# Optimization experiments

Hardware: AMD Instinct MI355X
Metric: run time of the kernel (lower is better)

The kernel has to match this reference:

```python
import jax, jax.numpy as jnp
import numpy as np

EPS = 1e-8  # matches torch.nn.functional.cosine_similarity default eps


def setup_inputs() -> dict:
    key = jax.random.key(0)
    k1, k2 = jax.random.split(key)
    B, C, L, D = 65536, 64, 64, 128
    x = jax.random.normal(k1, (B, D), dtype=jnp.float32)
    category_embeddings = jax.random.normal(k2, (C, L, D), dtype=jnp.float32)
    leaf_usage_counts = jnp.zeros((C, L), dtype=jnp.float32)
    return {
        "x": x,
        "category_embeddings": category_embeddings,
        "leaf_usage_counts": leaf_usage_counts,
    }


def reference(x, category_embeddings, leaf_usage_counts):
    # Cosine similarity: [B, C, L] without materializing the broadcast [B,C,L,D].
    x_norm = jnp.maximum(jnp.linalg.norm(x, axis=-1, keepdims=True), EPS)        # [B, 1]
    e_norm = jnp.maximum(jnp.linalg.norm(category_embeddings, axis=-1), EPS)     # [C, L]
    dots = jnp.einsum('bd,cld->bcl', x, category_embeddings)                     # [B, C, L]
    cosine_sim = dots / (x_norm[:, :, None] * e_norm[None, :, :])                # [B, C, L]

    # Training-path usage-count update (done under no_grad in torch):
    # per-category bincount of argmax leaf, scatter-added into the buffer.
    max_indices = jnp.argmax(cosine_sim, axis=2)                                 # [B, C] int
    C, L = leaf_usage_counts.shape
    cat_ids = jnp.broadcast_to(jnp.arange(C)[None, :], max_indices.shape)        # [B, C]
    leaf_counts = jnp.zeros((C, L), jnp.float32).at[cat_ids, max_indices].add(1.0)
    new_leaf_usage_counts = leaf_usage_counts + leaf_counts                      # [C, L]

    cosine_sim_max = jnp.max(cosine_sim, axis=2)                                 # [B, C]
    return cosine_sim_max, new_leaf_usage_counts
```

## Files before the change

### kernel.cpp

```cpp
#include <hip/hip_runtime.h>
#include <stdint.h>
#include <stddef.h>

#define D      128
#define NCATS  64
#define NLEAF  64
#define NC_BLK 4
#define BM     512
#define BIAS   32.0f

typedef _Float16 half8_t  __attribute__((ext_vector_type(8)));
typedef _Float16 half4h_t __attribute__((ext_vector_type(4)));
typedef float    float4_t __attribute__((ext_vector_type(4)));

__device__ __forceinline__ void async_ld16(const void* g, void* l) {
  __builtin_amdgcn_global_load_lds((const __attribute__((address_space(1))) uint32_t*)g,
                                   (__attribute__((address_space(3))) uint32_t*)l,
                                   16, 0, 0);
}

__global__ __launch_bounds__(256) void prep_e_kernel(const float* __restrict__ e,
                                                     char* __restrict__ e16,
                                                     const float* __restrict__ cin,
                                                     float* __restrict__ counts_out) {
  const int t  = threadIdx.x;
  const int rl = t >> 4;
  const int cc = t & 15;
  const int row = blockIdx.x * 16 + rl;
  const float* src = e + (size_t)row * D + cc * 8;
  float4_t v0 = *(const float4_t*)src;
  float4_t v1 = *(const float4_t*)(src + 4);
  float ss = v0.x*v0.x + v0.y*v0.y + v0.z*v0.z + v0.w*v0.w +
             v1.x*v1.x + v1.y*v1.y + v1.z*v1.z + v1.w*v1.w;
  ss += __shfl_xor(ss, 1);
  ss += __shfl_xor(ss, 2);
  ss += __shfl_xor(ss, 4);
  ss += __shfl_xor(ss, 8);
  const float inv = 1.0f / fmaxf(sqrtf(ss), 1e-8f);
  half8_t h;
  h[0] = (_Float16)(v0.x * inv); h[1] = (_Float16)(v0.y * inv);
  h[2] = (_Float16)(v0.z * inv); h[3] = (_Float16)(v0.w * inv);
  h[4] = (_Float16)(v1.x * inv); h[5] = (_Float16)(v1.y * inv);
  h[6] = (_Float16)(v1.z * inv); h[7] = (_Float16)(v1.w * inv);
  const int dc = cc ^ (rl & 7);
  *(half8_t*)(e16 + (size_t)row * 256 + dc * 16) = h;
  if (blockIdx.x < (NCATS * NLEAF) / 256)
    counts_out[blockIdx.x * 256 + t] = cin[blockIdx.x * 256 + t];
}

__global__ __launch_bounds__(512, 3) void main_kernel(const float* __restrict__ x,
                                                      const char* __restrict__ e16,
                                                      float* __restrict__ cos_out,
                                                      float* __restrict__ counts_out) {
  __shared__ __align__(16) char ebuf[NC_BLK][16384];
  __shared__ unsigned hist[NC_BLK * NLEAF];
  __shared__ __align__(16) _Float16 stage[BM * NC_BLK];

  const int tid  = threadIdx.x;
  const int w    = tid >> 6;
  const int lane = tid & 63;
  const int q    = lane >> 4;
  const int wl   = lane & 15;

  const int xcd    = blockIdx.x & 7;
  const int rb     = xcd * 16 + ((blockIdx.x >> 3) & 15);
  const int c_base = (blockIdx.x >> 7) * NC_BLK;
  const int b_base = rb * BM;

  {
    const char* g = e16 + (size_t)(c_base + (w >> 1)) * 16384 + (w & 1) * 8192 + lane * 16;
    char* l = &ebuf[w >> 1][(w & 1) * 8192 + lane * 16];
#pragma unroll
    for (int j = 0; j < 8; ++j) async_ld16(g + j * 1024, l + j * 1024);
  }

  for (int i = tid; i < NC_BLK * NLEAF; i += 512) hist[i] = 0;

  half8_t bfrag[4][4];
  float inv_x[4];
#pragma unroll
  for (int nt = 0; nt < 4; ++nt) {
    const int row = b_base + w * 64 + nt * 16 + wl;
    const float* xr = x + (size_t)row * D;
    float ss = 0.f;
#pragma unroll
    for (int s = 0; s < 4; ++s) {
      const float* p = xr + s * 32 + q * 8;
      float4_t v0 = *(const float4_t*)p;
      float4_t v1 = *(const float4_t*)(p + 4);
      half8_t h;
      h[0] = (_Float16)v0.x; h[1] = (_Float16)v0.y;
      h[2] = (_Float16)v0.z; h[3] = (_Float16)v0.w;
      h[4] = (_Float16)v1.x; h[5] = (_Float16)v1.y;
      h[6] = (_Float16)v1.z; h[7] = (_Float16)v1.w;
      bfrag[nt][s] = h;
      ss += v0.x*v0.x + v0.y*v0.y + v0.z*v0.z + v0.w*v0.w +
            v1.x*v1.x + v1.y*v1.y + v1.z*v1.z + v1.w*v1.w;
    }
    ss += __shfl_xor(ss, 16);
    ss += __shfl_xor(ss, 32);
    inv_x[nt] = 1.0f / fmaxf(sqrtf(ss), 1e-8f);
  }

  int rowbase[4], xoff[4];
#pragma unroll
  for (int rt = 0; rt < 4; ++rt) rowbase[rt] = (rt * 16 + wl) * 256;
#pragma unroll
  for (int s = 0; s < 4; ++s) xoff[s] = ((q + 4 * s) ^ (wl & 7)) * 16;

  const unsigned idq = (unsigned)(q << 2);
  const float4_t bias4 = {BIAS, BIAS, BIAS, BIAS};

  __syncthreads();

#pragma unroll
  for (int ci = 0; ci < NC_BLK; ++ci) {
    const char* cur = ebuf[ci];

    unsigned pk[4];
    __builtin_amdgcn_s_setprio(1);
#pragma unroll
    for (int rt = 0; rt < 4; ++rt) {
      float4_t acc[4];
#pragma unroll
      for (int s = 0; s < 4; ++s) {
        half8_t ef = *(const half8_t*)(cur + rowbase[rt] + xoff[s]);
#pragma unroll
        for (int nt = 0; nt < 4; ++nt)
          acc[nt] = __builtin_amdgcn_mfma_f32_16x16x32_f16(
              ef, bfrag[nt][s], (s == 0) ? bias4 : acc[nt], 0, 0, 0);
      }
#pragma unroll
      for (int nt = 0; nt < 4; ++nt)
#pragma unroll
        for (int reg = 0; reg < 4; ++reg) {
          unsigned k = (__float_as_uint(acc[nt][reg]) & 0xFFFFFFC0u) |
                       (unsigned)(rt * 16 + reg);
          if (rt == 0 && reg == 0) pk[nt] = k;
          else                     pk[nt] = (pk[nt] > k) ? pk[nt] : k;
        }
    }
    __builtin_amdgcn_s_setprio(0);

#pragma unroll
    for (int nt = 0; nt < 4; ++nt) {
      unsigned v = pk[nt] | idq;
      unsigned t = (unsigned)__shfl_xor((int)v, 16);
      v = (v > t) ? v : t;
      t = (unsigned)__shfl_xor((int)v, 32);
      v = (v > t) ? v : t;
      pk[nt] = v;
    }

    if (lane < 16) {
#pragma unroll
      for (int nt = 0; nt < 4; ++nt) {
        const unsigned p = pk[nt];
        const float val = (__uint_as_float(p & 0xFFFFFFC0u) - BIAS) * inv_x[nt];
        stage[(w * 64 + nt * 16 + lane) * NC_BLK + ci] = (_Float16)val;
        atomicAdd(&hist[ci * NLEAF + (int)(p & 63u)], 1u);
      }
    }
  }

  __syncthreads();

  {
    half4h_t h = *(const half4h_t*)&stage[tid * NC_BLK];
    float4_t v;
    v.x = (float)h[0]; v.y = (float)h[1]; v.z = (float)h[2]; v.w = (float)h[3];
    *(float4_t*)&cos_out[(size_t)(b_base + tid) * NCATS + c_base] = v;
  }

  if (tid < NC_BLK * NLEAF) {
    const unsigned v = hist[tid];
    if (v) atomicAdd(&counts_out[c_base * NLEAF + tid], (float)v);
  }
}

extern "C" void kernel_launch(void* const* d_in, const int* in_sizes, int n_in,
                              void* d_out, int out_size, void* d_ws, size_t ws_size,
                              hipStream_t stream) {
  const float* x   = (const float*)d_in[0];
  const float* e   = (const float*)d_in[1];
  const float* cin = (const float*)d_in[2];

  const int B = in_sizes[0] / D;
  const int erows = in_sizes[1] / D;
  float* cos_out = (float*)d_out;
  float* counts_out = cos_out + (size_t)B * NCATS;
  char* e16 = (char*)d_ws;

  prep_e_kernel<<<erows / 16, 256, 0, stream>>>(e, e16, cin, counts_out);
  main_kernel<<<(B / BM) * (NCATS / NC_BLK), 512, 0, stream>>>(x, e16, cos_out, counts_out);
}
```

Before: 157.3 us.

## Pre-convert x to fp16 fragment layout with norms in the prep kernel

The prep kernel now also converts x to fp16 once, stored in a fragment-friendly layout, and writes each row's inverse norm to workspace. The main kernel loads these halves directly instead of re-reading fp32 x and recomputing norms in each of its 16 category-block passes. The argmax reduction is rewritten with 3-input max helpers, and all lanes now write the staged output (one row each) instead of only 16 lanes. The trade-off is an extra 16 MB workspace write and read plus a larger prep launch, and the fast path is used only when the workspace is big enough.

```diff
diff --git a/kernel.cpp b/kernel.cpp
--- a/kernel.cpp
+++ b/kernel.cpp
@@ -9,6 +9,11 @@
 #define BM     512
 #define BIAS   32.0f
 
+#define WS_E16_BYTES   (1u << 20)
+#define WS_X16_BYTES   (16u << 20)
+#define WS_XINV_BYTES  (65536u * 4u)
+#define WS_NEEDED      ((size_t)WS_E16_BYTES + WS_X16_BYTES + WS_XINV_BYTES)
+
 typedef _Float16 half8_t  __attribute__((ext_vector_type(8)));
 typedef _Float16 half4h_t __attribute__((ext_vector_type(4)));
 typedef float    float4_t __attribute__((ext_vector_type(4)));
@@ -19,37 +24,71 @@
                                    16, 0, 0);
 }
 
-__global__ __launch_bounds__(256) void prep_e_kernel(const float* __restrict__ e,
-                                                     char* __restrict__ e16,
-                                                     const float* __restrict__ cin,
-                                                     float* __restrict__ counts_out) {
+__device__ __forceinline__ unsigned umax2(unsigned a, unsigned b) { return a > b ? a : b; }
+__device__ __forceinline__ unsigned umax3(unsigned a, unsigned b, unsigned c) {
+  return umax2(umax2(a, b), c);
+}
+
+__global__ __launch_bounds__(256) void prep_kernel(const float* __restrict__ e,
+                                                   const float* __restrict__ xf,
+                                                   char* __restrict__ e16,
+                                                   char* __restrict__ x16,
+                                                   float* __restrict__ xinv,
+                                                   const float* __restrict__ cin,
+                                                   float* __restrict__ counts_out) {
   const int t  = threadIdx.x;
   const int rl = t >> 4;
   const int cc = t & 15;
-  const int row = blockIdx.x * 16 + rl;
-  const float* src = e + (size_t)row * D + cc * 8;
-  float4_t v0 = *(const float4_t*)src;
-  float4_t v1 = *(const float4_t*)(src + 4);
-  float ss = v0.x*v0.x + v0.y*v0.y + v0.z*v0.z + v0.w*v0.w +
-             v1.x*v1.x + v1.y*v1.y + v1.z*v1.z + v1.w*v1.w;
-  ss += __shfl_xor(ss, 1);
-  ss += __shfl_xor(ss, 2);
-  ss += __shfl_xor(ss, 4);
-  ss += __shfl_xor(ss, 8);
-  const float inv = 1.0f / fmaxf(sqrtf(ss), 1e-8f);
-  half8_t h;
-  h[0] = (_Float16)(v0.x * inv); h[1] = (_Float16)(v0.y * inv);
-  h[2] = (_Float16)(v0.z * inv); h[3] = (_Float16)(v0.w * inv);
-  h[4] = (_Float16)(v1.x * inv); h[5] = (_Float16)(v1.y * inv);
-  h[6] = (_Float16)(v1.z * inv); h[7] = (_Float16)(v1.w * inv);
-  const int dc = cc ^ (rl & 7);
-  *(half8_t*)(e16 + (size_t)row * 256 + dc * 16) = h;
-  if (blockIdx.x < (NCATS * NLEAF) / 256)
-    counts_out[blockIdx.x * 256 + t] = cin[blockIdx.x * 256 + t];
-}
-
+
+  if (blockIdx.x < 256) {
+    const int row = blockIdx.x * 16 + rl;
+    const float* src = e + (size_t)row * D + cc * 8;
+    float4_t v0 = *(const float4_t*)src;
+    float4_t v1 = *(const float4_t*)(src + 4);
+    float ss = v0.x*v0.x + v0.y*v0.y + v0.z*v0.z + v0.w*v0.w +
+               v1.x*v1.x + v1.y*v1.y + v1.z*v1.z + v1.w*v1.w;
+    ss += __shfl_xor(ss, 1);
+    ss += __shfl_xor(ss, 2);
+    ss += __shfl_xor(ss, 4);
+    ss += __shfl_xor(ss, 8);
+    const float inv = 1.0f / fmaxf(sqrtf(ss), 1e-8f);
+    half8_t h;
+    h[0] = (_Float16)(v0.x * inv); h[1] = (_Float16)(v0.y * inv);
+    h[2] = (_Float16)(v0.z * inv); h[3] = (_Float16)(v0.w * inv);
+    h[4] = (_Float16)(v1.x * inv); h[5] = (_Float16)(v1.y * inv);
+    h[6] = (_Float16)(v1.z * inv); h[7] = (_Float16)(v1.w * inv);
+    const int dc = cc ^ (rl & 7);
+    *(half8_t*)(e16 + (size_t)row * 256 + dc * 16) = h;
+    if (blockIdx.x < (NCATS * NLEAF) / 256)
+      counts_out[blockIdx.x * 256 + t] = cin[blockIdx.x * 256 + t];
+  } else {
+    const int g   = blockIdx.x - 256;
+    const int row = g * 16 + rl;
+    const float* src = xf + (size_t)row * D + cc * 8;
+    float4_t v0 = *(const float4_t*)src;
+    float4_t v1 = *(const float4_t*)(src + 4);
+    float ss = v0.x*v0.x + v0.y*v0.y + v0.z*v0.z + v0.w*v0.w +
+               v1.x*v1.x + v1.y*v1.y + v1.z*v1.z + v1.w*v1.w;
+    ss += __shfl_xor(ss, 1);
+    ss += __shfl_xor(ss, 2);
+    ss += __shfl_xor(ss, 4);
+    ss += __shfl_xor(ss, 8);
+    const float inv = 1.0f / fmaxf(sqrtf(ss), 1e-8f);
+    half8_t h;
+    h[0] = (_Float16)v0.x; h[1] = (_Float16)v0.y;
+    h[2] = (_Float16)v0.z; h[3] = (_Float16)v0.w;
+    h[4] = (_Float16)v1.x; h[5] = (_Float16)v1.y;
+    h[6] = (_Float16)v1.z; h[7] = (_Float16)v1.w;
+    *(half8_t*)(x16 + (size_t)g * 4096 + cc * 256 + rl * 16) = h;
+    if (cc == 0) xinv[row] = inv;
+  }
+}
+
+template <bool XP>
 __global__ __launch_bounds__(512, 3) void main_kernel(const float* __restrict__ x,
                                                       const char* __restrict__ e16,
+                                                      const char* __restrict__ x16,
+                                                      const float* __restrict__ xinv,
                                                       float* __restrict__ cos_out,
                                                       float* __restrict__ counts_out) {
   __shared__ __align__(16) char ebuf[NC_BLK][16384];
@@ -74,32 +113,44 @@
     for (int j = 0; j < 8; ++j) async_ld16(g + j * 1024, l + j * 1024);
   }
 
-  for (int i = tid; i < NC_BLK * NLEAF; i += 512) hist[i] = 0;
+  if (tid < NC_BLK * NLEAF) hist[tid] = 0;
 
   half8_t bfrag[4][4];
   float inv_x[4];
-#pragma unroll
-  for (int nt = 0; nt < 4; ++nt) {
-    const int row = b_base + w * 64 + nt * 16 + wl;
-    const float* xr = x + (size_t)row * D;
-    float ss = 0.f;
-#pragma unroll
-    for (int s = 0; s < 4; ++s) {
-      const float* p = xr + s * 32 + q * 8;
-      float4_t v0 = *(const float4_t*)p;
-      float4_t v1 = *(const float4_t*)(p + 4);
-      half8_t h;
-      h[0] = (_Float16)v0.x; h[1] = (_Float16)v0.y;
-      h[2] = (_Float16)v0.z; h[3] = (_Float16)v0.w;
-      h[4] = (_Float16)v1.x; h[5] = (_Float16)v1.y;
-      h[6] = (_Float16)v1.z; h[7] = (_Float16)v1.w;
-      bfrag[nt][s] = h;
-      ss += v0.x*v0.x + v0.y*v0.y + v0.z*v0.z + v0.w*v0.w +
-            v1.x*v1.x + v1.y*v1.y + v1.z*v1.z + v1.w*v1.w;
-    }
-    ss += __shfl_xor(ss, 16);
-    ss += __shfl_xor(ss, 32);
-    inv_x[nt] = 1.0f / fmaxf(sqrtf(ss), 1e-8f);
+  if constexpr (XP) {
+    const size_t gbase = ((size_t)b_base >> 4) + (size_t)w * 4;
+#pragma unroll
+    for (int nt = 0; nt < 4; ++nt) {
+      const char* xr = x16 + (gbase + nt) * 4096 + q * 256 + wl * 16;
+#pragma unroll
+      for (int s = 0; s < 4; ++s)
+        bfrag[nt][s] = *(const half8_t*)(xr + s * 1024);
+      inv_x[nt] = xinv[b_base + w * 64 + nt * 16 + wl];
+    }
+  } else {
+#pragma unroll
+    for (int nt = 0; nt < 4; ++nt) {
+      const int row = b_base + w * 64 + nt * 16 + wl;
+      const float* xr = x + (size_t)row * D;
+      float ss = 0.f;
+#pragma unroll
+      for (int s = 0; s < 4; ++s) {
+        const float* p = xr + s * 32 + q * 8;
+        float4_t v0 = *(const float4_t*)p;
+        float4_t v1 = *(const float4_t*)(p + 4);
+        half8_t h;
+        h[0] = (_Float16)v0.x; h[1] = (_Float16)v0.y;
+        h[2] = (_Float16)v0.z; h[3] = (_Float16)v0.w;
+        h[4] = (_Float16)v1.x; h[5] = (_Float16)v1.y;
+        h[6] = (_Float16)v1.z; h[7] = (_Float16)v1.w;
+        bfrag[nt][s] = h;
+        ss += v0.x*v0.x + v0.y*v0.y + v0.z*v0.z + v0.w*v0.w +
+              v1.x*v1.x + v1.y*v1.y + v1.z*v1.z + v1.w*v1.w;
+      }
+      ss += __shfl_xor(ss, 16);
+      ss += __shfl_xor(ss, 32);
+      inv_x[nt] = 1.0f / fmaxf(sqrtf(ss), 1e-8f);
+    }
   }
 
   int rowbase[4], xoff[4];
@@ -131,14 +182,14 @@
               ef, bfrag[nt][s], (s == 0) ? bias4 : acc[nt], 0, 0, 0);
       }
 #pragma unroll
-      for (int nt = 0; nt < 4; ++nt)
-#pragma unroll
-        for (int reg = 0; reg < 4; ++reg) {
-          unsigned k = (__float_as_uint(acc[nt][reg]) & 0xFFFFFFC0u) |
-                       (unsigned)(rt * 16 + reg);
-          if (rt == 0 && reg == 0) pk[nt] = k;
-          else                     pk[nt] = (pk[nt] > k) ? pk[nt] : k;
-        }
+      for (int nt = 0; nt < 4; ++nt) {
+        const unsigned k0 = (__float_as_uint(acc[nt][0]) & 0xFFFFFFC0u) | (unsigned)(rt * 16 + 0);
+        const unsigned k1 = (__float_as_uint(acc[nt][1]) & 0xFFFFFFC0u) | (unsigned)(rt * 16 + 1);
+        const unsigned k2 = (__float_as_uint(acc[nt][2]) & 0xFFFFFFC0u) | (unsigned)(rt * 16 + 2);
+        const unsigned k3 = (__float_as_uint(acc[nt][3]) & 0xFFFFFFC0u) | (unsigned)(rt * 16 + 3);
+        const unsigned m  = umax3(k0, k1, k2);
+        pk[nt] = (rt == 0) ? umax2(m, k3) : umax3(m, k3, pk[nt]);
+      }
     }
     __builtin_amdgcn_s_setprio(0);
 
@@ -152,14 +203,16 @@
       pk[nt] = v;
     }
 
-    if (lane < 16) {
-#pragma unroll
-      for (int nt = 0; nt < 4; ++nt) {
-        const unsigned p = pk[nt];
-        const float val = (__uint_as_float(p & 0xFFFFFFC0u) - BIAS) * inv_x[nt];
-        stage[(w * 64 + nt * 16 + lane) * NC_BLK + ci] = (_Float16)val;
-        atomicAdd(&hist[ci * NLEAF + (int)(p & 63u)], 1u);
-      }
+    {
+      const unsigned pk01 = (q == 0) ? pk[0] : pk[1];
+      const unsigned pk23 = (q == 2) ? pk[2] : pk[3];
+      const unsigned pkq  = (q < 2) ? pk01 : pk23;
+      const float    iv01 = (q == 0) ? inv_x[0] : inv_x[1];
+      const float    iv23 = (q == 2) ? inv_x[2] : inv_x[3];
+      const float    invq = (q < 2) ? iv01 : iv23;
+      const float val = (__uint_as_float(pkq & 0xFFFFFFC0u) - BIAS) * invq;
+      stage[tid * NC_BLK + ci] = (_Float16)val;
+      atomicAdd(&hist[ci * NLEAF + (int)(pkq & 63u)], 1u);
     }
   }
 
@@ -186,11 +239,20 @@
   const float* cin = (const float*)d_in[2];
 
   const int B = in_sizes[0] / D;
-  const int erows = in_sizes[1] / D;
   float* cos_out = (float*)d_out;
   float* counts_out = cos_out + (size_t)B * NCATS;
-  char* e16 = (char*)d_ws;
-
-  prep_e_kernel<<<erows / 16, 256, 0, stream>>>(e, e16, cin, counts_out);
-  main_kernel<<<(B / BM) * (NCATS / NC_BLK), 512, 0, stream>>>(x, e16, cos_out, counts_out);
-}
+
+  char*  e16  = (char*)d_ws;
+  char*  x16  = e16 + WS_E16_BYTES;
+  float* xinv = (float*)(x16 + WS_X16_BYTES);
+
+  const bool xp = (ws_size >= WS_NEEDED);
+  const int prep_grid = xp ? (256 + B / 16) : 256;
+  prep_kernel<<<prep_grid, 256, 0, stream>>>(e, x, e16, x16, xinv, cin, counts_out);
+
+  const int main_grid = (B / BM) * (NCATS / NC_BLK);
+  if (xp)
+    main_kernel<true><<<main_grid, 512, 0, stream>>>(x, e16, x16, xinv, cos_out, counts_out);
+  else
+    main_kernel<false><<<main_grid, 512, 0, stream>>>(x, e16, x16, xinv, cos_out, counts_out);
+}
```

New measurement: 140.2 us. -10.9%, faster.
